# Kernel optimization log

Measured on AMD Instinct MI355X. Metric: run time of the kernel, lower is better.

## Reference

```python
import jax, jax.numpy as jnp
import numpy as np

B, Cin, Cout, H, W = 8, 64, 128, 128, 128
K, S, P = 3, 1, 1
KK = K * K
EPS = 1e-5


def _conv2d(x, w, b=None):
    out = jax.lax.conv_general_dilated(
        x, w, window_strides=(S, S), padding=[(P, P), (P, P)],
        dimension_numbers=('NCHW', 'OIHW', 'NCHW'))
    if b is not None:
        out = out + b[None, :, None, None]
    return out


def setup_inputs() -> dict:
    key = jax.random.key(0)
    k = jax.random.split(key, 5)
    sc = 1.0 / np.sqrt(Cin * KK)
    return {
        'x': jax.random.normal(k[0], (B, Cin, H, W), jnp.float32),
        'offset_w': jax.random.normal(k[1], (2 * KK, Cin, K, K), jnp.float32) * sc,
        'offset_b': jnp.zeros((2 * KK,), jnp.float32),
        'mask_w': jax.random.normal(k[2], (KK, Cin, K, K), jnp.float32) * sc,
        'mask_b': jnp.zeros((KK,), jnp.float32),
        'conv_w': jax.random.normal(k[3], (Cout, Cin, K, K), jnp.float32) * sc,
    }


def _deform_conv2d(x, offset, mask, w):
    """Modulated deformable conv (torchvision deform_conv2d semantics)."""
    Bn, C, Hh, Ww = x.shape
    Ho, Wo = offset.shape[2], offset.shape[3]
    off = offset.reshape(Bn, KK, 2, Ho, Wo)  # (y, x) pairs per kernel tap
    ky, kx = jnp.meshgrid(jnp.arange(K), jnp.arange(K), indexing='ij')
    ky = ky.reshape(KK).astype(x.dtype)
    kx = kx.reshape(KK).astype(x.dtype)
    hy = (jnp.arange(Ho) * S - P).astype(x.dtype)
    wx = (jnp.arange(Wo) * S - P).astype(x.dtype)
    # sampling positions [B, KK, Ho, Wo]
    py = off[:, :, 0] + ky[None, :, None, None] + hy[None, None, :, None]
    px = off[:, :, 1] + kx[None, :, None, None] + wx[None, None, None, :]

    y0 = jnp.floor(py)
    x0 = jnp.floor(px)
    wy1 = py - y0; wx1 = px - x0
    wy0 = 1.0 - wy1; wx0 = 1.0 - wx1

    xf = x.reshape(Bn, C, Hh * Ww)

    def gather(yi, xi):
        valid = ((yi >= 0) & (yi < Hh) & (xi >= 0) & (xi < Ww)).astype(x.dtype)
        yc = jnp.clip(yi, 0, Hh - 1).astype(jnp.int32)
        xc = jnp.clip(xi, 0, Ww - 1).astype(jnp.int32)
        idx = (yc * Ww + xc).reshape(Bn, -1)  # [B, KK*Ho*Wo]
        vals = jnp.take_along_axis(xf, idx[:, None, :], axis=2)  # [B, C, KK*Ho*Wo]
        return vals.reshape(Bn, C, KK, Ho, Wo) * valid.reshape(Bn, 1, KK, Ho, Wo)

    v = (gather(y0, x0) * (wy0 * wx0)[:, None]
         + gather(y0, x0 + 1) * (wy0 * wx1)[:, None]
         + gather(y0 + 1, x0) * (wy1 * wx0)[:, None]
         + gather(y0 + 1, x0 + 1) * (wy1 * wx1)[:, None])  # [B, C, KK, Ho, Wo]
    v = v * mask[:, None]  # modulation
    return jnp.einsum('bckhw,ock->bohw', v, w.reshape(w.shape[0], C, KK))


def reference(x, offset_w, offset_b, mask_w, mask_b, conv_w):
    offset = _conv2d(x, offset_w, offset_b)
    mask = jax.nn.sigmoid(_conv2d(x, mask_w, mask_b))
    out = _deform_conv2d(x, offset, mask, conv_w)
    # BatchNorm2d(affine=False), training-mode normalization over (N, H, W)
    mean = out.mean(axis=(0, 2, 3), keepdims=True)
    var = out.var(axis=(0, 2, 3), keepdims=True)
    return jax.nn.relu((out - mean) * jax.lax.rsqrt(var + EPS))
```

## Files before the change

### kernel.cpp

```cpp
#include <hip/hip_runtime.h>
#include <hip/hip_bf16.h>

#define H_ 128
#define W_ 128
#define HW 16384
#define CIN 64
#define COUT 128
#define KK9 9
#define BATCH 8
#define NPIX (BATCH * HW)
#define KDIM 576

typedef short bf16x8 __attribute__((ext_vector_type(8)));
typedef float f32x4  __attribute__((ext_vector_type(4)));
typedef unsigned short ushort_t;

union U4B { uint4 u; bf16x8 v; };

__device__ __forceinline__ float us2f(unsigned short u) {
    unsigned int v = ((unsigned int)u) << 16;
    float f;
    __builtin_memcpy(&f, &v, 4);
    return f;
}
__device__ __forceinline__ float lo_f(unsigned int w) {
    unsigned int v = w << 16;
    float f;
    __builtin_memcpy(&f, &v, 4);
    return f;
}
__device__ __forceinline__ float hi_f(unsigned int w) {
    unsigned int v = w & 0xffff0000u;
    float f;
    __builtin_memcpy(&f, &v, 4);
    return f;
}
__device__ __forceinline__ unsigned short f2us_bf(float f) {
    __hip_bfloat16 h = __float2bfloat16(f);
    unsigned short u;
    __builtin_memcpy(&u, &h, 2);
    return u;
}
__device__ __forceinline__ unsigned int pack2(float a, float b) {
    return (unsigned int)f2us_bf(a) | ((unsigned int)f2us_bf(b) << 16);
}

template <bool F32>
__device__ __forceinline__ float ld_in(const void* p, long i) {
    if (F32) return ((const float*)p)[i];
    return us2f(((const unsigned short*)p)[i]);
}

__global__ void detect_zero(const uint4* __restrict__ xr4,
                            float* __restrict__ flag,
                            float* __restrict__ gstat) {
    int t = threadIdx.x;
#pragma unroll
    for (int i = 0; i < 16; ++i) gstat[i * 256 + t] = 0.0f;
    if (t < 64) {
        uint4 v = xr4[t];
        unsigned int w[4] = {v.x, v.y, v.z, v.w};
        int big = 0;
#pragma unroll
        for (int q = 0; q < 4; ++q) {
            big += (((w[q] >> 7)  & 0xFF) >= 0xC0);
            big += (((w[q] >> 23) & 0xFF) >= 0xC0);
        }
        unsigned long long m = __ballot(big > 0);
        if (t == 0) flag[0] = m ? 1.0f : 0.0f;
    }
}

template <bool F32>
__device__ __forceinline__ void prep_body(const void* offw, const void* offb,
                                          const void* maskw, const void* maskb,
                                          const void* convw,
                                          ushort_t* wTs, ushort_t* wcats,
                                          float* bias, int i) {
    if (i < 73728) {
        int j = i & 7, lane = (i >> 3) & 63, n = (i >> 9) & 7, ks = i >> 12;
        int co = n * 16 + (lane & 15);
        int k  = ks * 32 + ((lane >> 4) << 3) + j;
        int kk = k >> 6, ci = k & 63;
        wTs[i] = f2us_bf(ld_in<F32>(convw, (long)co * KDIM + ci * 9 + kk));
    } else if (i < 73728 + 18432) {
        int i2 = i - 73728;
        int j = i2 & 7, lane = (i2 >> 3) & 63, n = (i2 >> 9) & 1, ks = i2 >> 10;
        int co2 = n * 16 + (lane & 15);
        int k   = ks * 32 + ((lane >> 4) << 3) + j;
        int kk = k >> 6, ci = k & 63;
        float v = 0.0f;
        if (co2 < 18)      v = ld_in<F32>(offw,  (long)co2 * KDIM + ci * 9 + kk);
        else if (co2 < 27) v = ld_in<F32>(maskw, (long)(co2 - 18) * KDIM + ci * 9 + kk);
        wcats[i2] = f2us_bf(v);
    } else if (i < 73728 + 18432 + 32) {
        int j = i - 73728 - 18432;
        float v = 0.0f;
        if (j < 18)      v = ld_in<F32>(offb, j);
        else if (j < 27) v = ld_in<F32>(maskb, j - 18);
        bias[j] = v;
    }
}

__global__ void prep_weights(const void* __restrict__ offw,
                             const void* __restrict__ offb,
                             const void* __restrict__ maskw,
                             const void* __restrict__ maskb,
                             const void* __restrict__ convw,
                             const float* __restrict__ flag,
                             ushort_t* __restrict__ wTs,
                             ushort_t* __restrict__ wcats,
                             float* __restrict__ bias) {
    int i = blockIdx.x * 256 + threadIdx.x;
    if (flag[0] != 0.0f)
        prep_body<true>(offw, offb, maskw, maskb, convw, wTs, wcats, bias, i);
    else
        prep_body<false>(offw, offb, maskw, maskb, convw, wTs, wcats, bias, i);
}

template <bool F32>
__device__ __forceinline__ void transpose_body(const void* x, ushort_t* xnb) {
    __shared__ float tile[CIN][64 + 1];
    int blk  = blockIdx.x;
    int b    = blk >> 8;
    int pix0 = (blk & 255) * 64;
    int t    = threadIdx.x;
    int lane = t & 63;
    int grp  = t >> 6;
#pragma unroll
    for (int r = 0; r < 16; ++r) {
        int ci = r * 4 + grp;
        tile[ci][lane] = ld_in<F32>(x, (long)(b * CIN + ci) * HW + pix0 + lane);
    }
    __syncthreads();
#pragma unroll
    for (int r = 0; r < 16; ++r) {
        int px = r * 4 + grp;
        xnb[(size_t)(b * HW + pix0 + px) * CIN + lane] = f2us_bf(tile[lane][px]);
    }
}

__global__ __launch_bounds__(256) void transpose_x(const void* __restrict__ x,
                                                   const float* __restrict__ flag,
                                                   ushort_t* __restrict__ xnb) {
    if (flag[0] != 0.0f) transpose_body<true>(x, xnb);
    else                 transpose_body<false>(x, xnb);
}

__global__ __launch_bounds__(1024, 4) void conv_mfma(
        const ushort_t* __restrict__ xnb,
        const ushort_t* __restrict__ wcats,
        const float* __restrict__ bias,
        float* __restrict__ off2,
        float* __restrict__ mask_ws) {
    __shared__ uint4 ldsB4[2304];

    int t    = threadIdx.x;
    int pix0 = blockIdx.x * 256;
    int b    = pix0 >> 14;
    int rem0 = pix0 & 16383;

    const uint4* ws4 = (const uint4*)wcats;
#pragma unroll
    for (int i = t; i < 2304; i += 1024) ldsB4[i] = ws4[i];

    int wave = t >> 6, lane = t & 63, mrow = lane & 15, quad = lane >> 4;
    int px_l = wave * 16 + mrow;
    int remp = rem0 + px_l;
    int yp = remp >> 7, xp = remp & 127;
    const ushort_t* xb = xnb + (size_t)b * HW * CIN + quad * 8;

    uint4 af0[9], af1[9];
#pragma unroll
    for (int kk = 0; kk < 9; ++kk) {
        int yy = yp + kk / 3 - 1;
        int xq = xp + kk % 3 - 1;
        bool ok = (yy >= 0) && (yy < H_) && (xq >= 0) && (xq < W_);
        const ushort_t* src = xb + (size_t)(yy * W_ + xq) * CIN;
        af0[kk] = ok ? *(const uint4*)src        : make_uint4(0, 0, 0, 0);
        af1[kk] = ok ? *(const uint4*)(src + 32) : make_uint4(0, 0, 0, 0);
    }
    __syncthreads();

    f32x4 acc[2];
    acc[0] = (f32x4){0.f, 0.f, 0.f, 0.f};
    acc[1] = (f32x4){0.f, 0.f, 0.f, 0.f};
    const ushort_t* ldsB = (const ushort_t*)ldsB4;
#pragma unroll
    for (int kk = 0; kk < 9; ++kk) {
#pragma unroll
        for (int half = 0; half < 2; ++half) {
            int ks = kk * 2 + half;
            U4B a; a.u = half ? af1[kk] : af0[kk];
#pragma unroll
            for (int n = 0; n < 2; ++n) {
                bf16x8 bf = *(const bf16x8*)(ldsB + ((ks * 2 + n) * 64 + lane) * 8);
                acc[n] = __builtin_amdgcn_mfma_f32_16x16x32_bf16(a.v, bf, acc[n], 0, 0, 0);
            }
        }
    }

#pragma unroll
    for (int n = 0; n < 2; ++n) {
        int co2 = n * 16 + mrow;
        if (co2 >= 27) continue;
        float bs = bias[co2];
#pragma unroll
        for (int r = 0; r < 4; ++r) {
            int px = wave * 16 + quad * 4 + r;
            float v = acc[n][r] + bs;
            if (co2 < 18) {
                off2[((size_t)(b * 9 + (co2 >> 1)) * HW + rem0 + px) * 2 + (co2 & 1)] = v;
            } else {
                mask_ws[(size_t)(b * 9 + (co2 - 18)) * HW + rem0 + px] =
                    1.0f / (1.0f + __expf(-v));
            }
        }
    }
}

__device__ __forceinline__ void issue_tap(int yp_t, int xp_t,
                                          float oy, float ox, float mk,
                                          const ushort_t* __restrict__ xb,
                                          uint4* cb, float* wg) {
    float py  = (float)yp_t + oy;
    float pxf = (float)xp_t + ox;
    float y0f = floorf(py), x0f = floorf(pxf);
    int yi = (int)y0f, xi = (int)x0f;
    float wy1 = py - y0f, wx1 = pxf - x0f;
    float wy0 = 1.0f - wy1, wx0 = 1.0f - wx1;
    int ya  = min(max(yi, 0), H_ - 1);
    int yb  = min(max(yi + 1, 0), H_ - 1);
    int xa  = min(max(xi, 0), W_ - 1);
    int xb2 = min(max(xi + 1, 0), W_ - 1);
    bool vy0 = (yi >= 0) & (yi < H_);
    bool vy1 = (yi >= -1) & (yi < H_ - 1);
    bool vx0 = (xi >= 0) & (xi < W_);
    bool vx1 = (xi >= -1) & (xi < W_ - 1);
    float m0 = mk * wy0, m1 = mk * wy1;
    wg[0] = (vy0 & vx0) ? m0 * wx0 : 0.0f;
    wg[1] = (vy0 & vx1) ? m0 * wx1 : 0.0f;
    wg[2] = (vy1 & vx0) ? m1 * wx0 : 0.0f;
    wg[3] = (vy1 & vx1) ? m1 * wx1 : 0.0f;
    int ra = ya << 13, rb = yb << 13;
    int ca = xa << 6,  cb_ = xb2 << 6;
    const ushort_t* s00 = xb + (ra + ca);
    const ushort_t* s01 = xb + (ra + cb_);
    const ushort_t* s10 = xb + (rb + ca);
    const ushort_t* s11 = xb + (rb + cb_);
    cb[0] = *(const uint4*)s00;
    cb[1] = *(const uint4*)(s00 + 32);
    cb[2] = *(const uint4*)s01;
    cb[3] = *(const uint4*)(s01 + 32);
    cb[4] = *(const uint4*)s10;
    cb[5] = *(const uint4*)(s10 + 32);
    cb[6] = *(const uint4*)s11;
    cb[7] = *(const uint4*)(s11 + 32);
}

__device__ __forceinline__ void consume_tap(int kk, const uint4* cb,
                                            const float* wg,
                                            const ushort_t* __restrict__ ldsB,
                                            int lane, f32x4* acc) {
    float2 v2[8];
#pragma unroll
    for (int j = 0; j < 8; ++j) v2[j] = make_float2(0.f, 0.f);
#pragma unroll
    for (int c = 0; c < 4; ++c) {
        float w = wg[c];
        unsigned int ww[8] = {cb[2 * c].x,     cb[2 * c].y,
                              cb[2 * c].z,     cb[2 * c].w,
                              cb[2 * c + 1].x, cb[2 * c + 1].y,
                              cb[2 * c + 1].z, cb[2 * c + 1].w};
#pragma unroll
        for (int j = 0; j < 8; ++j) {
            v2[j].x = fmaf(w, lo_f(ww[j]), v2[j].x);
            v2[j].y = fmaf(w, hi_f(ww[j]), v2[j].y);
        }
    }
    unsigned int w8[8];
#pragma unroll
    for (int j = 0; j < 8; ++j)
        w8[j] = pack2(v2[j].x, v2[j].y);
    U4B a0, a1;
    a0.u = make_uint4(w8[0], w8[1], w8[2], w8[3]);
    a1.u = make_uint4(w8[4], w8[5], w8[6], w8[7]);
#pragma unroll
    for (int half = 0; half < 2; ++half) {
        int ks = kk * 2 + half;
        U4B a = half ? a1 : a0;
        const ushort_t* bbase = ldsB + ((size_t)(ks * 8) * 64 + lane) * 8;
#pragma unroll
        for (int n = 0; n < 8; ++n) {
            bf16x8 bf = *(const bf16x8*)(bbase + n * 64 * 8);
            acc[n] = __builtin_amdgcn_mfma_f32_16x16x32_bf16(a.v, bf, acc[n], 0, 0, 0);
        }
    }
}

__global__ __launch_bounds__(1024, 4) void deform_mfma(
        const ushort_t* __restrict__ xnb,
        const float* __restrict__ off2,
        const float* __restrict__ mask_ws,
        const ushort_t* __restrict__ wTs,
        ushort_t* __restrict__ prebn,
        float* __restrict__ gstat) {
    __shared__ uint4 ldsB4[9216];
    __shared__ float red[256];

    int t    = threadIdx.x;
    int pix0 = blockIdx.x * 256;
    int b    = pix0 >> 14;
    int rem0 = pix0 & 16383;

    const uint4* ws4 = (const uint4*)wTs;
#pragma unroll
    for (int i = 0; i < 9; ++i) ldsB4[i * 1024 + t] = ws4[i * 1024 + t];
    if (t < 256) red[t] = 0.0f;

    int wave = t >> 6, lane = t & 63, mrow = lane & 15, quad = lane >> 4;
    int px_l = wave * 16 + mrow;
    int remp = rem0 + px_l;
    int yp = remp >> 7, xp = remp & 127;
    const ushort_t* xb = xnb + (size_t)b * HW * CIN + quad * 8;
    size_t obase = (size_t)b * 9 * HW + remp;

    float2 o0 = *(const float2*)(off2 + obase * 2);
    float2 o1 = *(const float2*)(off2 + (obase + HW) * 2);
    float mk0 = mask_ws[obase];
    float mk1 = mask_ws[obase + HW];
    __syncthreads();

    f32x4 acc[8];
#pragma unroll
    for (int n = 0; n < 8; ++n) acc[n] = (f32x4){0.f, 0.f, 0.f, 0.f};
    const ushort_t* ldsB = (const ushort_t*)ldsB4;

    uint4 cb0[8], cb1[8];
    float wg0[4], wg1[4];
    issue_tap(yp - 1, xp - 1, o0.x, o0.y, mk0, xb, cb0, wg0);
    __builtin_amdgcn_sched_barrier(0);
#pragma unroll
    for (int kk = 0; kk < 9; ++kk) {
        if ((kk & 1) == 0) {
            if (kk < 7) {
                o0  = *(const float2*)(off2 + (obase + (size_t)(kk + 2) * HW) * 2);
                mk0 = mask_ws[obase + (size_t)(kk + 2) * HW];
            }
            if (kk < 8)
                issue_tap(yp + (kk + 1) / 3 - 1, xp + (kk + 1) % 3 - 1,
                          o1.x, o1.y, mk1, xb, cb1, wg1);
            __builtin_amdgcn_sched_barrier(0);
            consume_tap(kk, cb0, wg0, ldsB, lane, acc);
        } else {
            if (kk < 7) {
                o1  = *(const float2*)(off2 + (obase + (size_t)(kk + 2) * HW) * 2);
                mk1 = mask_ws[obase + (size_t)(kk + 2) * HW];
            }
            if (kk < 8)
                issue_tap(yp + (kk + 1) / 3 - 1, xp + (kk + 1) % 3 - 1,
                          o0.x, o0.y, mk0, xb, cb0, wg0);
            __builtin_amdgcn_sched_barrier(0);
            consume_tap(kk, cb1, wg1, ldsB, lane, acc);
        }
    }

#pragma unroll
    for (int n = 0; n < 8; ++n) {
        int co = n * 16 + mrow;
        float s = 0.f, ss = 0.f;
#pragma unroll
        for (int r = 0; r < 4; ++r) {
            int pg = pix0 + wave * 16 + quad * 4 + r;
            float v = acc[n][r];
            prebn[(size_t)pg * COUT + co] = f2us_bf(v);
            s += v;
            ss += v * v;
        }
        s  += __shfl_xor(s, 16, 64);
        s  += __shfl_xor(s, 32, 64);
        ss += __shfl_xor(ss, 16, 64);
        ss += __shfl_xor(ss, 32, 64);
        if (quad == 0) {
            atomicAdd(&red[co], s);
            atomicAdd(&red[128 + co], ss);
        }
    }
    __syncthreads();
    if (t < 256) atomicAdd(&gstat[(blockIdx.x & 15) * 256 + t], red[t]);
}

__global__ __launch_bounds__(256) void bn_apply_t(const ushort_t* __restrict__ prebn,
                                                  const float* __restrict__ gstat,
                                                  float* __restrict__ out) {
    __shared__ float tile[128 * 65];
    __shared__ float mvs[256];
    int t = threadIdx.x;
    if (t < 128) {
        float s = 0.f, ss = 0.f;
#pragma unroll
        for (int part = 0; part < 16; ++part) {
            s  += gstat[part * 256 + t];
            ss += gstat[part * 256 + 128 + t];
        }
        const float invN = 1.0f / (float)NPIX;
        float mean = s * invN;
        float var  = ss * invN - mean * mean;
        if (!isfinite(mean)) mean = 0.0f;
        float r = rsqrtf(fmaxf(var, 0.0f) + 1e-5f);
        if (!isfinite(r)) r = 1.0f;
        mvs[t]       = mean;
        mvs[128 + t] = r;
    }
    __syncthreads();
    int pix0 = blockIdx.x * 64;
    int b    = pix0 >> 14;
    int rem0 = pix0 & 16383;
    const ushort_t* src = prebn + (size_t)pix0 * COUT;
#pragma unroll
    for (int r = 0; r < 32; ++r) {
        int i = r * 256 + t;
        int p = i >> 7, c = i & 127;
        float v = us2f(src[i]);
        v = fmaxf((v - mvs[c]) * mvs[128 + c], 0.0f);
        tile[c * 65 + p] = v;
    }
    __syncthreads();
#pragma unroll
    for (int r = 0; r < 32; ++r) {
        int i = r * 256 + t;
        int c2 = i >> 6, p2 = i & 63;
        out[(size_t)(b * COUT + c2) * HW + rem0 + p2] = tile[c2 * 65 + p2];
    }
}

extern "C" void kernel_launch(void* const* d_in, const int* in_sizes, int n_in,
                              void* d_out, int out_size, void* d_ws, size_t ws_size,
                              hipStream_t stream) {
    (void)in_sizes; (void)n_in; (void)out_size; (void)ws_size;
    const void* x     = d_in[0];
    const void* offw  = d_in[1];
    const void* offb  = d_in[2];
    const void* maskw = d_in[3];
    const void* maskb = d_in[4];
    const void* convw = d_in[5];

    float* ws       = (float*)d_ws;
    float* off2     = ws;
    float* mask_ws  = off2 + 2359296;
    float* bias     = mask_ws + 1179648;
    float* gstat    = bias + 32;
    float* flag     = gstat + 4096;
    ushort_t* wTs   = (ushort_t*)(flag + 16);
    ushort_t* wcats = wTs + 73728;
    ushort_t* xnb   = wcats + 18432;
    ushort_t* prebn = xnb + 8388608;
    float* out      = (float*)d_out;

    detect_zero<<<1, 256, 0, stream>>>((const uint4*)x, flag, gstat);
    prep_weights<<<361, 256, 0, stream>>>(offw, offb, maskw, maskb, convw, flag, wTs, wcats, bias);
    transpose_x<<<2048, 256, 0, stream>>>(x, flag, xnb);
    conv_mfma<<<512, 1024, 0, stream>>>(xnb, wcats, bias, off2, mask_ws);
    deform_mfma<<<512, 1024, 0, stream>>>(xnb, off2, mask_ws, wTs, prebn, gstat);
    bn_apply_t<<<2048, 256, 0, stream>>>(prebn, gstat, out);
}
```

Baseline: 232.6 us.

## Pipeline deformable gather at half-tap granularity to cut register pressure

Splits each tap's bilinear gather into two 32-channel halves. Each half issues its four loads one stage ahead of the matching MFMA consumption. The double buffer of gathered values shrinks from 16 uint4 registers to 8, which should ease VGPR pressure under the 1024-thread launch bounds and allow finer overlap of loads with MFMA work. The trade-off is a shorter prefetch distance, which may leave global-load latency less well hidden.

```diff
diff --git a/kernel.cpp b/kernel.cpp
--- a/kernel.cpp
+++ b/kernel.cpp
@@ -219,10 +219,9 @@
     }
 }
 
-__device__ __forceinline__ void issue_tap(int yp_t, int xp_t,
-                                          float oy, float ox, float mk,
-                                          const ushort_t* __restrict__ xb,
-                                          uint4* cb, float* wg) {
+__device__ __forceinline__ void compute_tap(int yp_t, int xp_t,
+                                            float oy, float ox, float mk,
+                                            int* ofs, float* wg) {
     float py  = (float)yp_t + oy;
     float pxf = (float)xp_t + ox;
     float y0f = floorf(py), x0f = floorf(pxf);
@@ -244,57 +243,42 @@
     wg[3] = (vy1 & vx1) ? m1 * wx1 : 0.0f;
     int ra = ya << 13, rb = yb << 13;
     int ca = xa << 6,  cb_ = xb2 << 6;
-    const ushort_t* s00 = xb + (ra + ca);
-    const ushort_t* s01 = xb + (ra + cb_);
-    const ushort_t* s10 = xb + (rb + ca);
-    const ushort_t* s11 = xb + (rb + cb_);
-    cb[0] = *(const uint4*)s00;
-    cb[1] = *(const uint4*)(s00 + 32);
-    cb[2] = *(const uint4*)s01;
-    cb[3] = *(const uint4*)(s01 + 32);
-    cb[4] = *(const uint4*)s10;
-    cb[5] = *(const uint4*)(s10 + 32);
-    cb[6] = *(const uint4*)s11;
-    cb[7] = *(const uint4*)(s11 + 32);
-}
-
-__device__ __forceinline__ void consume_tap(int kk, const uint4* cb,
-                                            const float* wg,
-                                            const ushort_t* __restrict__ ldsB,
-                                            int lane, f32x4* acc) {
-    float2 v2[8];
-#pragma unroll
-    for (int j = 0; j < 8; ++j) v2[j] = make_float2(0.f, 0.f);
+    ofs[0] = ra + ca;  ofs[1] = ra + cb_;
+    ofs[2] = rb + ca;  ofs[3] = rb + cb_;
+}
+
+__device__ __forceinline__ void issue_half(const ushort_t* __restrict__ xb,
+                                           const int* ofs, int hoff, uint4* cb) {
+#pragma unroll
+    for (int c = 0; c < 4; ++c)
+        cb[c] = *(const uint4*)(xb + ofs[c] + hoff);
+}
+
+__device__ __forceinline__ void consume_half(int ks, const uint4* cb,
+                                             const float* wg,
+                                             const ushort_t* __restrict__ ldsB,
+                                             int lane, f32x4* acc) {
+    float2 v2[4];
+#pragma unroll
+    for (int j = 0; j < 4; ++j) v2[j] = make_float2(0.f, 0.f);
 #pragma unroll
     for (int c = 0; c < 4; ++c) {
         float w = wg[c];
-        unsigned int ww[8] = {cb[2 * c].x,     cb[2 * c].y,
-                              cb[2 * c].z,     cb[2 * c].w,
-                              cb[2 * c + 1].x, cb[2 * c + 1].y,
-                              cb[2 * c + 1].z, cb[2 * c + 1].w};
-#pragma unroll
-        for (int j = 0; j < 8; ++j) {
+        unsigned int ww[4] = {cb[c].x, cb[c].y, cb[c].z, cb[c].w};
+#pragma unroll
+        for (int j = 0; j < 4; ++j) {
             v2[j].x = fmaf(w, lo_f(ww[j]), v2[j].x);
             v2[j].y = fmaf(w, hi_f(ww[j]), v2[j].y);
         }
     }
-    unsigned int w8[8];
-#pragma unroll
-    for (int j = 0; j < 8; ++j)
-        w8[j] = pack2(v2[j].x, v2[j].y);
-    U4B a0, a1;
-    a0.u = make_uint4(w8[0], w8[1], w8[2], w8[3]);
-    a1.u = make_uint4(w8[4], w8[5], w8[6], w8[7]);
-#pragma unroll
-    for (int half = 0; half < 2; ++half) {
-        int ks = kk * 2 + half;
-        U4B a = half ? a1 : a0;
-        const ushort_t* bbase = ldsB + ((size_t)(ks * 8) * 64 + lane) * 8;
-#pragma unroll
-        for (int n = 0; n < 8; ++n) {
-            bf16x8 bf = *(const bf16x8*)(bbase + n * 64 * 8);
-            acc[n] = __builtin_amdgcn_mfma_f32_16x16x32_bf16(a.v, bf, acc[n], 0, 0, 0);
-        }
+    U4B a;
+    a.u = make_uint4(pack2(v2[0].x, v2[0].y), pack2(v2[1].x, v2[1].y),
+                     pack2(v2[2].x, v2[2].y), pack2(v2[3].x, v2[3].y));
+    const ushort_t* bbase = ldsB + ((size_t)(ks * 8) * 64 + lane) * 8;
+#pragma unroll
+    for (int n = 0; n < 8; ++n) {
+        bf16x8 bf = *(const bf16x8*)(bbase + n * 64 * 8);
+        acc[n] = __builtin_amdgcn_mfma_f32_16x16x32_bf16(a.v, bf, acc[n], 0, 0, 0);
     }
 }
 
@@ -325,10 +309,10 @@
     const ushort_t* xb = xnb + (size_t)b * HW * CIN + quad * 8;
     size_t obase = (size_t)b * 9 * HW + remp;
 
-    float2 o0 = *(const float2*)(off2 + obase * 2);
-    float2 o1 = *(const float2*)(off2 + (obase + HW) * 2);
-    float mk0 = mask_ws[obase];
-    float mk1 = mask_ws[obase + HW];
+    float2 oE = *(const float2*)(off2 + obase * 2);
+    float2 oO = *(const float2*)(off2 + (obase + HW) * 2);
+    float mkE = mask_ws[obase];
+    float mkO = mask_ws[obase + HW];
     __syncthreads();
 
     f32x4 acc[8];
@@ -336,33 +320,41 @@
     for (int n = 0; n < 8; ++n) acc[n] = (f32x4){0.f, 0.f, 0.f, 0.f};
     const ushort_t* ldsB = (const ushort_t*)ldsB4;
 
-    uint4 cb0[8], cb1[8];
-    float wg0[4], wg1[4];
-    issue_tap(yp - 1, xp - 1, o0.x, o0.y, mk0, xb, cb0, wg0);
+    int   ofs[2][4];
+    float wg[2][4];
+    uint4 cb[2][4];
+
+    compute_tap(yp - 1, xp - 1, oE.x, oE.y, mkE, ofs[0], wg[0]);
+    issue_half(xb, ofs[0], 0, cb[0]);
     __builtin_amdgcn_sched_barrier(0);
-#pragma unroll
-    for (int kk = 0; kk < 9; ++kk) {
-        if ((kk & 1) == 0) {
+
+#pragma unroll
+    for (int hs = 0; hs < 18; ++hs) {
+        const int kk = hs >> 1;
+        const int h  = hs & 1;
+        const int tp = kk & 1;
+        const int bp = hs & 1;
+        if (h == 0) {
+            issue_half(xb, ofs[tp], 32, cb[bp ^ 1]);
+        } else {
+            if (kk < 8) {
+                const int nt = kk + 1;
+                float ooy = (nt & 1) ? oO.x : oE.x;
+                float oox = (nt & 1) ? oO.y : oE.y;
+                float omk = (nt & 1) ? mkO : mkE;
+                compute_tap(yp + nt / 3 - 1, xp + nt % 3 - 1, ooy, oox, omk,
+                            ofs[tp ^ 1], wg[tp ^ 1]);
+                issue_half(xb, ofs[tp ^ 1], 0, cb[bp ^ 1]);
+            }
             if (kk < 7) {
-                o0  = *(const float2*)(off2 + (obase + (size_t)(kk + 2) * HW) * 2);
-                mk0 = mask_ws[obase + (size_t)(kk + 2) * HW];
+                const int pt = kk + 2;
+                float2 o = *(const float2*)(off2 + (obase + (size_t)pt * HW) * 2);
+                float  m = mask_ws[obase + (size_t)pt * HW];
+                if (tp) { oO = o; mkO = m; } else { oE = o; mkE = m; }
             }
-            if (kk < 8)
-                issue_tap(yp + (kk + 1) / 3 - 1, xp + (kk + 1) % 3 - 1,
-                          o1.x, o1.y, mk1, xb, cb1, wg1);
-            __builtin_amdgcn_sched_barrier(0);
-            consume_tap(kk, cb0, wg0, ldsB, lane, acc);
-        } else {
-            if (kk < 7) {
-                o1  = *(const float2*)(off2 + (obase + (size_t)(kk + 2) * HW) * 2);
-                mk1 = mask_ws[obase + (size_t)(kk + 2) * HW];
-            }
-            if (kk < 8)
-                issue_tap(yp + (kk + 1) / 3 - 1, xp + (kk + 1) % 3 - 1,
-                          o0.x, o0.y, mk0, xb, cb0, wg0);
-            __builtin_amdgcn_sched_barrier(0);
-            consume_tap(kk, cb1, wg1, ldsB, lane, acc);
-        }
+        }
+        __builtin_amdgcn_sched_barrier(0);
+        consume_half(hs, cb[bp], wg[tp], ldsB, lane, acc);
     }
 
 #pragma unroll
```

Result: faster. 219.8 us (-5.5%).
